# Kernel tuning notes

Measured on AMD Instinct MI355X. Metric: run time of the kernel, lower is better.

Reference implementation:

```python
import jax, jax.numpy as jnp
import numpy as np

D_MODEL = 1024
N_HEADS = 16
HEAD_DIM = D_MODEL // N_HEADS
B, S = 2, 2048


def setup_inputs() -> dict:
    key = jax.random.key(0)
    ks = jax.random.split(key, 12)
    sd = 1.0 / np.sqrt(D_MODEL)
    inp = {
        "x": jax.random.normal(ks[0], (B, S, D_MODEL), dtype=jnp.float32),
        "rel_bias": jax.random.normal(ks[1], (N_HEADS, S, S), dtype=jnp.float32) * 0.02,
        "attn_mask": jnp.zeros((1, 1, S, S), dtype=jnp.float32),
        # Linear params in torch layout: W [out, in], b [out]
        "Wq": jax.random.normal(ks[2], (D_MODEL, D_MODEL), dtype=jnp.float32) * sd,
        "bq": jnp.zeros((D_MODEL,), dtype=jnp.float32),
        "Wk": jax.random.normal(ks[3], (D_MODEL, D_MODEL), dtype=jnp.float32) * sd,
        "bk": jnp.zeros((D_MODEL,), dtype=jnp.float32),
        "Wv": jax.random.normal(ks[4], (D_MODEL, D_MODEL), dtype=jnp.float32) * sd,
        "bv": jnp.zeros((D_MODEL,), dtype=jnp.float32),
        "Wo": jax.random.normal(ks[5], (D_MODEL, D_MODEL), dtype=jnp.float32) * sd,
        "bo": jnp.zeros((D_MODEL,), dtype=jnp.float32),
    }
    return inp


def _split_heads(t):
    # [B, S, D] -> [B, H, S, Hd]
    b, s, _ = t.shape
    return t.reshape(b, s, N_HEADS, HEAD_DIM).transpose(0, 2, 1, 3)


def reference(x, rel_bias, attn_mask, Wq, bq, Wk, bk, Wv, bv, Wo, bo):
    scale = HEAD_DIM ** (-0.5)
    q = _split_heads(x @ Wq.T + bq)  # [B, H, S, Hd]
    k = _split_heads(x @ Wk.T + bk)
    v = _split_heads(x @ Wv.T + bv)
    scores = jnp.einsum("bhqd,bhkd->bhqk", q, k) * scale
    scores = scores + rel_bias  # [H,S,S] broadcasts over batch
    scores = scores + attn_mask  # [1,1,S,S]
    probs = jax.nn.softmax(scores, axis=-1)
    ctx = jnp.einsum("bhqk,bhkd->bhqd", probs, v)  # [B, H, S, Hd]
    ctx = ctx.transpose(0, 2, 1, 3).reshape(x.shape[0], x.shape[1], D_MODEL)
    return ctx @ Wo.T + bo
```

## Files before the change

kernel.cpp:

```cpp
#include <hip/hip_runtime.h>
#include <hip/hip_bf16.h>
#include <stdint.h>

#define S_LEN 2048
#define DM 1024
#define NH 16
#define HD 64

typedef __bf16 bf16x8 __attribute__((ext_vector_type(8)));
typedef float f32x4 __attribute__((ext_vector_type(4)));
typedef unsigned short u16x4 __attribute__((ext_vector_type(4)));

#if __has_builtin(__builtin_amdgcn_exp2f)
#define EXP2F(x) __builtin_amdgcn_exp2f(x)
#else
#define EXP2F(x) exp2f(x)
#endif

__device__ __forceinline__ unsigned short f2bf(float f){
  union { float f; uint32_t u; } v; v.f = f;
  uint32_t r = v.u + 0x7fffu + ((v.u >> 16) & 1u);
  return (unsigned short)(r >> 16);
}

__device__ __forceinline__ void load_lds16(const void* g, void* l){
  __builtin_amdgcn_global_load_lds((const __attribute__((address_space(1))) void*)g,
                                   (__attribute__((address_space(3))) void*)l, 16, 0, 0);
}

__device__ __forceinline__ f32x4 mfma16(bf16x8 a, bf16x8 b, f32x4 c){
  return __builtin_amdgcn_mfma_f32_16x16x32_bf16(a, b, c, 0, 0, 0);
}

__device__ __forceinline__ bf16x8 lds_swz_read(const unsigned short* base, int row, int cb){
  int addr = (row << 7) + (cb ^ ((row & 7) << 4));
  return *reinterpret_cast<const bf16x8*>(reinterpret_cast<const char*>(base) + addr);
}

__global__ void prep_kernel(const float* __restrict__ x,
                            const float* __restrict__ wq, const float* __restrict__ wk,
                            const float* __restrict__ wv, const float* __restrict__ wo,
                            unsigned short* __restrict__ ws_base){
  long idx = ((long)blockIdx.x * 256 + threadIdx.x) * 4;
  const float* s; unsigned short* d; long off;
  if (idx < (1L << 22)) { s = x; d = ws_base; off = idx; }
  else {
    long r = idx - (1L << 22);
    int wsel = (int)(r >> 20);
    off = r & ((1L << 20) - 1);
    s = wsel == 0 ? wq : wsel == 1 ? wk : wsel == 2 ? wv : wo;
    d = ws_base + (1L << 22) + ((long)wsel << 20);
  }
  float4 f = *reinterpret_cast<const float4*>(s + off);
  u16x4 o;
  o[0] = f2bf(f.x); o[1] = f2bf(f.y); o[2] = f2bf(f.z); o[3] = f2bf(f.w);
  *reinterpret_cast<u16x4*>(d + off) = o;
}

template<int MODE>
__global__ __launch_bounds__(256, 2)
void gemm_bt_kernel(const unsigned short* __restrict__ A,
                    const unsigned short* __restrict__ B0,
                    const unsigned short* __restrict__ B1,
                    const unsigned short* __restrict__ B2,
                    const float* __restrict__ bias0,
                    const float* __restrict__ bias1,
                    const float* __restrict__ bias2,
                    unsigned short* __restrict__ q_out,
                    unsigned short* __restrict__ k_out,
                    unsigned short* __restrict__ vt_out,
                    float* __restrict__ f_out)
{
  __shared__ unsigned short As[128 * 64];
  __shared__ unsigned short Bs[128 * 64];
  const int tid = threadIdx.x;
  const int lane = tid & 63;
  const int w = tid >> 6;
  const int wr = w >> 1, wc = w & 1;
  const int mBase = blockIdx.y * 128;
  int nb = blockIdx.x;
  const unsigned short* Bmat; const float* bias; int mat;
  if constexpr (MODE == 0) {
    mat = nb >> 3;
    nb &= 7;
    Bmat = mat == 0 ? B0 : (mat == 1 ? B1 : B2);
    bias = mat == 0 ? bias0 : (mat == 1 ? bias1 : bias2);
  } else { mat = 0; Bmat = B0; bias = bias0; }
  const int nBase = nb * 128;

  f32x4 acc[4][4] = {};
  const int srow = lane >> 3;
  const int ksrc = ((lane & 7) ^ srow) * 8;
  const unsigned short* ArowBase = A    + (size_t)(mBase + w * 32 + srow) * DM + ksrc;
  const unsigned short* BrowBase = Bmat + (size_t)(nBase + w * 32 + srow) * DM + ksrc;

  for (int kt = 0; kt < 16; ++kt) {
    #pragma unroll
    for (int i = 0; i < 4; ++i) {
      load_lds16(ArowBase + (size_t)(i * 8) * DM + kt * 64, &As[(w * 4 + i) * 512]);
      load_lds16(BrowBase + (size_t)(i * 8) * DM + kt * 64, &Bs[(w * 4 + i) * 512]);
    }
    __syncthreads();
    #pragma unroll
    for (int kk = 0; kk < 2; ++kk) {
      bf16x8 af[4], bfr[4];
      const int cb = kk * 64 + ((lane >> 4) << 4);
      #pragma unroll
      for (int m = 0; m < 4; ++m)
        af[m] = lds_swz_read(As, wr * 64 + m * 16 + (lane & 15), cb);
      #pragma unroll
      for (int n = 0; n < 4; ++n)
        bfr[n] = lds_swz_read(Bs, wc * 64 + n * 16 + (lane & 15), cb);
      #pragma unroll
      for (int m = 0; m < 4; ++m)
        #pragma unroll
        for (int n = 0; n < 4; ++n)
          acc[m][n] = mfma16(af[m], bfr[n], acc[m][n]);
    }
    __syncthreads();
  }

  #pragma unroll
  for (int m = 0; m < 4; ++m) {
    #pragma unroll
    for (int n = 0; n < 4; ++n) {
      const int col = nBase + wc * 64 + n * 16 + (lane & 15);
      const float bv = bias[col];
      const int row0 = mBase + wr * 64 + m * 16 + ((lane >> 4) << 2);
      if constexpr (MODE == 1) {
        #pragma unroll
        for (int j = 0; j < 4; ++j)
          f_out[(size_t)(row0 + j) * DM + col] = acc[m][n][j] + bv;
      } else {
        const int h = col >> 6, d = col & 63;
        if (mat < 2) {
          unsigned short* dst = (mat == 0) ? q_out : k_out;
          #pragma unroll
          for (int j = 0; j < 4; ++j) {
            const int row = row0 + j;
            const int b = row >> 11, s = row & 2047;
            dst[(((size_t)b * NH + h) * S_LEN + s) * HD + d] = f2bf(acc[m][n][j] + bv);
          }
        } else {
          const int b = row0 >> 11, s = row0 & 2047;
          u16x4 pk;
          #pragma unroll
          for (int j = 0; j < 4; ++j) pk[j] = f2bf(acc[m][n][j] + bv);
          *reinterpret_cast<u16x4*>(&vt_out[(((size_t)b * NH + h) * HD + d) * S_LEN + s]) = pk;
        }
      }
    }
  }
}


#define LOAD_RAW(kvB) do {                                                    \
    rb0 = *reinterpret_cast<const f32x4*>(bp + (kvB) + g * 4);                \
    rm0 = *reinterpret_cast<const f32x4*>(mp + (kvB) + g * 4);                \
    rb1 = *reinterpret_cast<const f32x4*>(bp + (kvB) + 16 + g * 4);           \
    rm1 = *reinterpret_cast<const f32x4*>(mp + (kvB) + 16 + g * 4);           \
    rb2 = *reinterpret_cast<const f32x4*>(bp + (kvB) + 32 + g * 4);           \
    rm2 = *reinterpret_cast<const f32x4*>(mp + (kvB) + 32 + g * 4);           \
    rb3 = *reinterpret_cast<const f32x4*>(bp + (kvB) + 48 + g * 4);           \
    rm3 = *reinterpret_cast<const f32x4*>(mp + (kvB) + 48 + g * 4);           \
  } while (0)

#define COMBINE do {                                                          \
    bm0 = (rb0 + rm0) * L2E; bm1 = (rb1 + rm1) * L2E;                         \
    bm2 = (rb2 + rm2) * L2E; bm3 = (rb3 + rm3) * L2E;                         \
  } while (0)

#define STAGE(kvB, buf) do {                                                                \
    load_lds16(Kp + (size_t)((kvB) + w * 16 + srow) * HD + ksrc,      &Ks[buf][(w * 2) * 512]);     \
    load_lds16(Vp + (size_t)(w * 16 + srow) * S_LEN + (kvB) + ksrc,   &Vs[buf][(w * 2) * 512]);     \
    load_lds16(Kp + (size_t)((kvB) + w * 16 + 8 + srow) * HD + ksrc,  &Ks[buf][(w * 2 + 1) * 512]); \
    load_lds16(Vp + (size_t)(w * 16 + 8 + srow) * S_LEN + (kvB) + ksrc, &Vs[buf][(w * 2 + 1) * 512]); \
  } while (0)

#define QK_COL(NN, SCN) do {                                                  \
    bf16x8 kf0_ = lds_swz_read(KSB_, (NN) * 16 + q, cbq);                     \
    bf16x8 kf1_ = lds_swz_read(KSB_, (NN) * 16 + q, 64 + cbq);                \
    f32x4 z_ = {};                                                            \
    z_ = mfma16(kf0_, qf0, z_);                                               \
    SCN = mfma16(kf1_, qf1, z_);                                              \
  } while (0)

#define BIAS_COL(SCN, BMN) do {                                               \
    SCN[0] = SCN[0] * SC + BMN[0];                                            \
    SCN[1] = SCN[1] * SC + BMN[1];                                            \
    SCN[2] = SCN[2] * SC + BMN[2];                                            \
    SCN[3] = SCN[3] * SC + BMN[3];                                            \
    mt_ = fmaxf(mt_, fmaxf(fmaxf(SCN[0], SCN[1]), fmaxf(SCN[2], SCN[3])));    \
  } while (0)

#define EXP_COL(SCN) do {                                                     \
    SCN[0] = EXP2F(SCN[0] - mn_); SCN[1] = EXP2F(SCN[1] - mn_);               \
    SCN[2] = EXP2F(SCN[2] - mn_); SCN[3] = EXP2F(SCN[3] - mn_);               \
  } while (0)

#define PWR_COL(NN, SCN) do {                                                 \
    u16x4 pk_;                                                                \
    pk_[0] = f2bf(SCN[0]); pk_[1] = f2bf(SCN[1]);                             \
    pk_[2] = f2bf(SCN[2]); pk_[3] = f2bf(SCN[3]);                             \
    const int colb_ = ((NN) * 16 + 4 * g) * 2;                                \
    *reinterpret_cast<u16x4*>(                                                \
        reinterpret_cast<char*>(Pw_) + (q << 7) + (colb_ ^ ((q & 7) << 4))) = pk_; \
  } while (0)

#define PV_COL(NN, ACCN) do {                                                 \
    bf16x8 vf0_ = lds_swz_read(VSB_, (NN) * 16 + q, cbq);                     \
    bf16x8 vf1_ = lds_swz_read(VSB_, (NN) * 16 + q, 64 + cbq);                \
    ACCN = mfma16(vf0_, pf0_, ACCN);                                          \
    ACCN = mfma16(vf1_, pf1_, ACCN);                                          \
  } while (0)

#define COMPUTE_TILE(KSB, VSB) do {                                           \
    const unsigned short* KSB_ = (KSB);                                       \
    const unsigned short* VSB_ = (VSB);                                       \
    f32x4 sc0_, sc1_, sc2_, sc3_;                                             \
    QK_COL(0, sc0_); QK_COL(1, sc1_); QK_COL(2, sc2_); QK_COL(3, sc3_);       \
    float mt_ = -3.0e38f;                                                     \
    BIAS_COL(sc0_, bm0); BIAS_COL(sc1_, bm1);                                 \
    BIAS_COL(sc2_, bm2); BIAS_COL(sc3_, bm3);                                 \
    mt_ = fmaxf(mt_, __shfl_xor(mt_, 16));                                    \
    mt_ = fmaxf(mt_, __shfl_xor(mt_, 32));                                    \
    const float mn_ = fmaxf(m_run, mt_);                                      \
    const float corr_ = EXP2F(m_run - mn_);                                   \
    m_run = mn_;                                                              \
    EXP_COL(sc0_); EXP_COL(sc1_); EXP_COL(sc2_); EXP_COL(sc3_);               \
    f32x4 ls4_ = sc0_ + sc1_ + sc2_ + sc3_;                                   \
    float ls_ = ls4_[0] + ls4_[1] + ls4_[2] + ls4_[3];                        \
    ls_ += __shfl_xor(ls_, 16);                                               \
    ls_ += __shfl_xor(ls_, 32);                                               \
    l_run = l_run * corr_ + ls_;                                              \
    acc0_ *= corr_; acc1_ *= corr_; acc2_ *= corr_; acc3_ *= corr_;           \
    unsigned short* Pw_ = Ps[w];                                              \
    PWR_COL(0, sc0_); PWR_COL(1, sc1_); PWR_COL(2, sc2_); PWR_COL(3, sc3_);   \
    bf16x8 pf0_ = lds_swz_read(Pw_, q, cbq);                                  \
    bf16x8 pf1_ = lds_swz_read(Pw_, q, 64 + cbq);                             \
    PV_COL(0, acc0_); PV_COL(1, acc1_); PV_COL(2, acc2_); PV_COL(3, acc3_);   \
  } while (0)

__global__ __launch_bounds__(256) __attribute__((amdgpu_waves_per_eu(3, 4)))
void attn_kernel(const unsigned short* __restrict__ Q,
                 const unsigned short* __restrict__ Kmat,
                 const unsigned short* __restrict__ Vt,
                 const float* __restrict__ rel_bias,
                 const float* __restrict__ mask,
                 unsigned short* __restrict__ ctx)
{
  __shared__ unsigned short Ks[2][64 * 64];
  __shared__ unsigned short Vs[2][64 * 64];
  __shared__ unsigned short Ps[4][16 * 64];

  const int logical = (blockIdx.x & 7) * 128 + (blockIdx.x >> 3);
  const int b  = logical & 1;
  const int qt = (logical >> 1) & 31;
  const int h  = logical >> 6;

  const int lane = threadIdx.x & 63, w = threadIdx.x >> 6;
  const int q = lane & 15, g = lane >> 4;
  const size_t bh = (size_t)b * NH + h;
  const int qRow = qt * 64 + w * 16;
  const unsigned short* Qp = Q + (bh * S_LEN + qRow) * HD;
  bf16x8 qf0 = *reinterpret_cast<const bf16x8*>(Qp + (size_t)q * HD + g * 8);
  bf16x8 qf1 = *reinterpret_cast<const bf16x8*>(Qp + (size_t)q * HD + 32 + g * 8);

  const unsigned short* Kp = Kmat + bh * (size_t)S_LEN * HD;
  const unsigned short* Vp = Vt + bh * (size_t)HD * S_LEN;
  const float* bp = rel_bias + (size_t)h * S_LEN * S_LEN + (size_t)(qRow + q) * S_LEN;
  const float* mp = mask + (size_t)(qRow + q) * S_LEN;

  float m_run = -3.0e38f, l_run = 0.f;
  f32x4 acc0_ = {}, acc1_ = {}, acc2_ = {}, acc3_ = {};
  f32x4 rb0, rb1, rb2, rb3, rm0, rm1, rm2, rm3;
  f32x4 bm0, bm1, bm2, bm3;

  const float SC  = 0.125f * 1.44269504089f;
  const float L2E = 1.44269504089f;

  const int srow = lane >> 3;
  const int ksrc = ((lane & 7) ^ srow) * 8;
  const int cbq = g << 4;

  LOAD_RAW(0);
  STAGE(0, 0);
  __syncthreads();

  for (int i = 0; i < 16; ++i) {
    const int t0 = 2 * i;
    COMBINE;
    LOAD_RAW((t0 + 1) * 64);
    STAGE((t0 + 1) * 64, 1);
    COMPUTE_TILE(Ks[0], Vs[0]);
    __syncthreads();
    COMBINE;
    if (i < 15) {
      LOAD_RAW((t0 + 2) * 64);
      STAGE((t0 + 2) * 64, 0);
    }
    COMPUTE_TILE(Ks[1], Vs[1]);
    __syncthreads();
  }

  const float inv = 1.0f / l_run;
  acc0_ *= inv; acc1_ *= inv; acc2_ *= inv; acc3_ *= inv;
  unsigned short* Pw_ = Ps[w];
  PWR_COL(0, acc0_); PWR_COL(1, acc1_); PWR_COL(2, acc2_); PWR_COL(3, acc3_);
  bf16x8 c0 = lds_swz_read(Pw_, q, g << 4);
  bf16x8 c1 = lds_swz_read(Pw_, q, 64 + (g << 4));
  unsigned short* cp = ctx + ((size_t)b * S_LEN + qRow + q) * DM + h * HD;
  *reinterpret_cast<bf16x8*>(cp + 8 * g) = c0;
  *reinterpret_cast<bf16x8*>(cp + 32 + 8 * g) = c1;
}

extern "C" void kernel_launch(void* const* d_in, const int* in_sizes, int n_in,
                              void* d_out, int out_size, void* d_ws, size_t ws_size,
                              hipStream_t stream) {
  (void)in_sizes; (void)n_in; (void)out_size; (void)ws_size;
  const float* x  = (const float*)d_in[0];
  const float* rb = (const float*)d_in[1];
  const float* mk = (const float*)d_in[2];
  const float* Wq = (const float*)d_in[3];
  const float* bq = (const float*)d_in[4];
  const float* Wk = (const float*)d_in[5];
  const float* bk = (const float*)d_in[6];
  const float* Wv = (const float*)d_in[7];
  const float* bv = (const float*)d_in[8];
  const float* Wo = (const float*)d_in[9];
  const float* bo = (const float*)d_in[10];
  float* out = (float*)d_out;

  unsigned short* ws  = (unsigned short*)d_ws;
  unsigned short* xb  = ws;
  unsigned short* wqb = ws + (1L << 22);
  unsigned short* wkb = wqb + (1L << 20);
  unsigned short* wvb = wkb + (1L << 20);
  unsigned short* wob = wvb + (1L << 20);
  unsigned short* Qw  = wob + (1L << 20);
  unsigned short* Kw  = Qw + (1L << 22);
  unsigned short* Vtw = Kw + (1L << 22);
  unsigned short* ctx = Vtw + (1L << 22);

  prep_kernel<<<8192, 256, 0, stream>>>(x, Wq, Wk, Wv, Wo, ws);
  gemm_bt_kernel<0><<<dim3(24, 32), 256, 0, stream>>>(
      xb, wqb, wkb, wvb, bq, bk, bv, Qw, Kw, Vtw, nullptr);
  attn_kernel<<<1024, 256, 0, stream>>>(Qw, Kw, Vtw, rb, mk, ctx);
  gemm_bt_kernel<1><<<dim3(8, 32), 256, 0, stream>>>(
      ctx, wob, nullptr, nullptr, bo, nullptr, nullptr, nullptr, nullptr, nullptr, out);
}
```

Baseline: 237.6 us.

## Load K and V fragments directly from global into registers, dropping LDS staging

Replaces the double-buffered LDS staging of K and V tiles, along with its block-wide barriers, with per-wave direct global loads of the MFMA operand fragments into registers, prefetched one tile ahead. This removes the LDS traffic and the __syncthreads from the KV loop and frees shared memory for occupancy. In exchange, each of the four waves now fetches the same K/V data separately from global/L2, which multiplies that traffic by four. It also raises register pressure and issues narrower, less coalesced loads.

```diff
diff --git a/kernel.cpp b/kernel.cpp
--- a/kernel.cpp
+++ b/kernel.cpp
@@ -170,19 +170,26 @@
     bm2 = (rb2 + rm2) * L2E; bm3 = (rb3 + rm3) * L2E;                         \
   } while (0)
 
-#define STAGE(kvB, buf) do {                                                                \
-    load_lds16(Kp + (size_t)((kvB) + w * 16 + srow) * HD + ksrc,      &Ks[buf][(w * 2) * 512]);     \
-    load_lds16(Vp + (size_t)(w * 16 + srow) * S_LEN + (kvB) + ksrc,   &Vs[buf][(w * 2) * 512]);     \
-    load_lds16(Kp + (size_t)((kvB) + w * 16 + 8 + srow) * HD + ksrc,  &Ks[buf][(w * 2 + 1) * 512]); \
-    load_lds16(Vp + (size_t)(w * 16 + 8 + srow) * S_LEN + (kvB) + ksrc, &Vs[buf][(w * 2 + 1) * 512]); \
-  } while (0)
-
-#define QK_COL(NN, SCN) do {                                                  \
-    bf16x8 kf0_ = lds_swz_read(KSB_, (NN) * 16 + q, cbq);                     \
-    bf16x8 kf1_ = lds_swz_read(KSB_, (NN) * 16 + q, 64 + cbq);                \
-    f32x4 z_ = {};                                                            \
-    z_ = mfma16(kf0_, qf0, z_);                                               \
-    SCN = mfma16(kf1_, qf1, z_);                                              \
+#define LOAD_K(kvB) do {                                                      \
+    kf00 = *reinterpret_cast<const bf16x8*>(Kq + (size_t)(kvB) * HD);         \
+    kf01 = *reinterpret_cast<const bf16x8*>(Kq + (size_t)(kvB) * HD + 32);    \
+    kf10 = *reinterpret_cast<const bf16x8*>(Kq + (size_t)(kvB) * HD + 1024);  \
+    kf11 = *reinterpret_cast<const bf16x8*>(Kq + (size_t)(kvB) * HD + 1056);  \
+    kf20 = *reinterpret_cast<const bf16x8*>(Kq + (size_t)(kvB) * HD + 2048);  \
+    kf21 = *reinterpret_cast<const bf16x8*>(Kq + (size_t)(kvB) * HD + 2080);  \
+    kf30 = *reinterpret_cast<const bf16x8*>(Kq + (size_t)(kvB) * HD + 3072);  \
+    kf31 = *reinterpret_cast<const bf16x8*>(Kq + (size_t)(kvB) * HD + 3104);  \
+  } while (0)
+
+#define LOAD_V(kvB) do {                                                      \
+    vf00 = *reinterpret_cast<const bf16x8*>(Vq0 + (kvB));                     \
+    vf01 = *reinterpret_cast<const bf16x8*>(Vq0 + (kvB) + 32);                \
+    vf10 = *reinterpret_cast<const bf16x8*>(Vq1 + (kvB));                     \
+    vf11 = *reinterpret_cast<const bf16x8*>(Vq1 + (kvB) + 32);                \
+    vf20 = *reinterpret_cast<const bf16x8*>(Vq2 + (kvB));                     \
+    vf21 = *reinterpret_cast<const bf16x8*>(Vq2 + (kvB) + 32);                \
+    vf30 = *reinterpret_cast<const bf16x8*>(Vq3 + (kvB));                     \
+    vf31 = *reinterpret_cast<const bf16x8*>(Vq3 + (kvB) + 32);                \
   } while (0)
 
 #define BIAS_COL(SCN, BMN) do {                                               \
@@ -205,40 +212,6 @@
     const int colb_ = ((NN) * 16 + 4 * g) * 2;                                \
     *reinterpret_cast<u16x4*>(                                                \
         reinterpret_cast<char*>(Pw_) + (q << 7) + (colb_ ^ ((q & 7) << 4))) = pk_; \
-  } while (0)
-
-#define PV_COL(NN, ACCN) do {                                                 \
-    bf16x8 vf0_ = lds_swz_read(VSB_, (NN) * 16 + q, cbq);                     \
-    bf16x8 vf1_ = lds_swz_read(VSB_, (NN) * 16 + q, 64 + cbq);                \
-    ACCN = mfma16(vf0_, pf0_, ACCN);                                          \
-    ACCN = mfma16(vf1_, pf1_, ACCN);                                          \
-  } while (0)
-
-#define COMPUTE_TILE(KSB, VSB) do {                                           \
-    const unsigned short* KSB_ = (KSB);                                       \
-    const unsigned short* VSB_ = (VSB);                                       \
-    f32x4 sc0_, sc1_, sc2_, sc3_;                                             \
-    QK_COL(0, sc0_); QK_COL(1, sc1_); QK_COL(2, sc2_); QK_COL(3, sc3_);       \
-    float mt_ = -3.0e38f;                                                     \
-    BIAS_COL(sc0_, bm0); BIAS_COL(sc1_, bm1);                                 \
-    BIAS_COL(sc2_, bm2); BIAS_COL(sc3_, bm3);                                 \
-    mt_ = fmaxf(mt_, __shfl_xor(mt_, 16));                                    \
-    mt_ = fmaxf(mt_, __shfl_xor(mt_, 32));                                    \
-    const float mn_ = fmaxf(m_run, mt_);                                      \
-    const float corr_ = EXP2F(m_run - mn_);                                   \
-    m_run = mn_;                                                              \
-    EXP_COL(sc0_); EXP_COL(sc1_); EXP_COL(sc2_); EXP_COL(sc3_);               \
-    f32x4 ls4_ = sc0_ + sc1_ + sc2_ + sc3_;                                   \
-    float ls_ = ls4_[0] + ls4_[1] + ls4_[2] + ls4_[3];                        \
-    ls_ += __shfl_xor(ls_, 16);                                               \
-    ls_ += __shfl_xor(ls_, 32);                                               \
-    l_run = l_run * corr_ + ls_;                                              \
-    acc0_ *= corr_; acc1_ *= corr_; acc2_ *= corr_; acc3_ *= corr_;           \
-    unsigned short* Pw_ = Ps[w];                                              \
-    PWR_COL(0, sc0_); PWR_COL(1, sc1_); PWR_COL(2, sc2_); PWR_COL(3, sc3_);   \
-    bf16x8 pf0_ = lds_swz_read(Pw_, q, cbq);                                  \
-    bf16x8 pf1_ = lds_swz_read(Pw_, q, 64 + cbq);                             \
-    PV_COL(0, acc0_); PV_COL(1, acc1_); PV_COL(2, acc2_); PV_COL(3, acc3_);   \
   } while (0)
 
 __global__ __launch_bounds__(256) __attribute__((amdgpu_waves_per_eu(3, 4)))
@@ -249,8 +222,6 @@
                  const float* __restrict__ mask,
                  unsigned short* __restrict__ ctx)
 {
-  __shared__ unsigned short Ks[2][64 * 64];
-  __shared__ unsigned short Vs[2][64 * 64];
   __shared__ unsigned short Ps[4][16 * 64];
 
   const int logical = (blockIdx.x & 7) * 128 + (blockIdx.x >> 3);
@@ -266,8 +237,12 @@
   bf16x8 qf0 = *reinterpret_cast<const bf16x8*>(Qp + (size_t)q * HD + g * 8);
   bf16x8 qf1 = *reinterpret_cast<const bf16x8*>(Qp + (size_t)q * HD + 32 + g * 8);
 
-  const unsigned short* Kp = Kmat + bh * (size_t)S_LEN * HD;
-  const unsigned short* Vp = Vt + bh * (size_t)HD * S_LEN;
+  const unsigned short* Kq  = Kmat + bh * (size_t)S_LEN * HD + (size_t)q * HD + g * 8;
+  const unsigned short* Vb  = Vt + bh * (size_t)HD * S_LEN + g * 8;
+  const unsigned short* Vq0 = Vb + (size_t)q * S_LEN;
+  const unsigned short* Vq1 = Vb + (size_t)(16 + q) * S_LEN;
+  const unsigned short* Vq2 = Vb + (size_t)(32 + q) * S_LEN;
+  const unsigned short* Vq3 = Vb + (size_t)(48 + q) * S_LEN;
   const float* bp = rel_bias + (size_t)h * S_LEN * S_LEN + (size_t)(qRow + q) * S_LEN;
   const float* mp = mask + (size_t)(qRow + q) * S_LEN;
 
@@ -275,37 +250,59 @@
   f32x4 acc0_ = {}, acc1_ = {}, acc2_ = {}, acc3_ = {};
   f32x4 rb0, rb1, rb2, rb3, rm0, rm1, rm2, rm3;
   f32x4 bm0, bm1, bm2, bm3;
+  bf16x8 kf00, kf01, kf10, kf11, kf20, kf21, kf30, kf31;
+  bf16x8 vf00, vf01, vf10, vf11, vf20, vf21, vf30, vf31;
 
   const float SC  = 0.125f * 1.44269504089f;
   const float L2E = 1.44269504089f;
-
-  const int srow = lane >> 3;
-  const int ksrc = ((lane & 7) ^ srow) * 8;
   const int cbq = g << 4;
+  unsigned short* Pw_ = Ps[w];
 
   LOAD_RAW(0);
-  STAGE(0, 0);
-  __syncthreads();
-
-  for (int i = 0; i < 16; ++i) {
-    const int t0 = 2 * i;
+  LOAD_K(0);
+  LOAD_V(0);
+
+  for (int t = 0; t < 32; ++t) {
+    const int nxt = (t + 1) * 64;
     COMBINE;
-    LOAD_RAW((t0 + 1) * 64);
-    STAGE((t0 + 1) * 64, 1);
-    COMPUTE_TILE(Ks[0], Vs[0]);
-    __syncthreads();
-    COMBINE;
-    if (i < 15) {
-      LOAD_RAW((t0 + 2) * 64);
-      STAGE((t0 + 2) * 64, 0);
-    }
-    COMPUTE_TILE(Ks[1], Vs[1]);
-    __syncthreads();
+    if (t < 31) LOAD_RAW(nxt);
+
+    f32x4 sc0_, sc1_, sc2_, sc3_;
+    { f32x4 z_ = {}; z_ = mfma16(kf00, qf0, z_); sc0_ = mfma16(kf01, qf1, z_); }
+    { f32x4 z_ = {}; z_ = mfma16(kf10, qf0, z_); sc1_ = mfma16(kf11, qf1, z_); }
+    { f32x4 z_ = {}; z_ = mfma16(kf20, qf0, z_); sc2_ = mfma16(kf21, qf1, z_); }
+    { f32x4 z_ = {}; z_ = mfma16(kf30, qf0, z_); sc3_ = mfma16(kf31, qf1, z_); }
+    if (t < 31) LOAD_K(nxt);
+
+    float mt_ = -3.0e38f;
+    BIAS_COL(sc0_, bm0); BIAS_COL(sc1_, bm1);
+    BIAS_COL(sc2_, bm2); BIAS_COL(sc3_, bm3);
+    mt_ = fmaxf(mt_, __shfl_xor(mt_, 16));
+    mt_ = fmaxf(mt_, __shfl_xor(mt_, 32));
+    const float mn_ = fmaxf(m_run, mt_);
+    const float corr_ = EXP2F(m_run - mn_);
+    m_run = mn_;
+    EXP_COL(sc0_); EXP_COL(sc1_); EXP_COL(sc2_); EXP_COL(sc3_);
+    f32x4 ls4_ = sc0_ + sc1_ + sc2_ + sc3_;
+    float ls_ = ls4_[0] + ls4_[1] + ls4_[2] + ls4_[3];
+    ls_ += __shfl_xor(ls_, 16);
+    ls_ += __shfl_xor(ls_, 32);
+    l_run = l_run * corr_ + ls_;
+    acc0_ *= corr_; acc1_ *= corr_; acc2_ *= corr_; acc3_ *= corr_;
+
+    PWR_COL(0, sc0_); PWR_COL(1, sc1_); PWR_COL(2, sc2_); PWR_COL(3, sc3_);
+    bf16x8 pf0_ = lds_swz_read(Pw_, q, cbq);
+    bf16x8 pf1_ = lds_swz_read(Pw_, q, 64 + cbq);
+
+    acc0_ = mfma16(vf00, pf0_, acc0_); acc0_ = mfma16(vf01, pf1_, acc0_);
+    acc1_ = mfma16(vf10, pf0_, acc1_); acc1_ = mfma16(vf11, pf1_, acc1_);
+    acc2_ = mfma16(vf20, pf0_, acc2_); acc2_ = mfma16(vf21, pf1_, acc2_);
+    acc3_ = mfma16(vf30, pf0_, acc3_); acc3_ = mfma16(vf31, pf1_, acc3_);
+    if (t < 31) LOAD_V(nxt);
   }
 
   const float inv = 1.0f / l_run;
   acc0_ *= inv; acc1_ *= inv; acc2_ *= inv; acc3_ *= inv;
-  unsigned short* Pw_ = Ps[w];
   PWR_COL(0, acc0_); PWR_COL(1, acc1_); PWR_COL(2, acc2_); PWR_COL(3, acc3_);
   bf16x8 c0 = lds_swz_read(Pw_, q, g << 4);
   bf16x8 c1 = lds_swz_read(Pw_, q, 64 + (g << 4));
```

New measurement: 431.7 us. +81.7%, slower.

## Deepen bias/mask prefetch to two tiles with explicit vmcnt waits and barriers

Applied to the files above, without the earlier changes.

Splits the bias and mask register prefetch into two alternating sets so the raw loads run two tiles ahead instead of one. The __syncthreads calls are replaced by partial s_waitcnt vmcnt(8) plus s_barrier, with sched_barrier fences, so the outstanding bias loads are not drained at every tile boundary. The final two tiles are peeled out of the loop. This adds 32 VGPRs of live prefetch state, which may hurt occupancy. Correctness now depends on the hand-counted vmcnt ordering, which assumes the LDS DMA loads are issued before the register loads.

```diff
diff --git a/kernel.cpp b/kernel.cpp
--- a/kernel.cpp
+++ b/kernel.cpp
@@ -154,35 +154,51 @@
 }
 
 
-#define LOAD_RAW(kvB) do {                                                    \
-    rb0 = *reinterpret_cast<const f32x4*>(bp + (kvB) + g * 4);                \
-    rm0 = *reinterpret_cast<const f32x4*>(mp + (kvB) + g * 4);                \
-    rb1 = *reinterpret_cast<const f32x4*>(bp + (kvB) + 16 + g * 4);           \
-    rm1 = *reinterpret_cast<const f32x4*>(mp + (kvB) + 16 + g * 4);           \
-    rb2 = *reinterpret_cast<const f32x4*>(bp + (kvB) + 32 + g * 4);           \
-    rm2 = *reinterpret_cast<const f32x4*>(mp + (kvB) + 32 + g * 4);           \
-    rb3 = *reinterpret_cast<const f32x4*>(bp + (kvB) + 48 + g * 4);           \
-    rm3 = *reinterpret_cast<const f32x4*>(mp + (kvB) + 48 + g * 4);           \
-  } while (0)
-
-#define COMBINE do {                                                          \
-    bm0 = (rb0 + rm0) * L2E; bm1 = (rb1 + rm1) * L2E;                         \
-    bm2 = (rb2 + rm2) * L2E; bm3 = (rb3 + rm3) * L2E;                         \
-  } while (0)
-
-#define STAGE(kvB, buf) do {                                                                \
-    load_lds16(Kp + (size_t)((kvB) + w * 16 + srow) * HD + ksrc,      &Ks[buf][(w * 2) * 512]);     \
-    load_lds16(Vp + (size_t)(w * 16 + srow) * S_LEN + (kvB) + ksrc,   &Vs[buf][(w * 2) * 512]);     \
-    load_lds16(Kp + (size_t)((kvB) + w * 16 + 8 + srow) * HD + ksrc,  &Ks[buf][(w * 2 + 1) * 512]); \
+#define WAITV8 do { asm volatile("s_waitcnt vmcnt(8)" ::: "memory"); } while (0)
+#define WAITV0 do { asm volatile("s_waitcnt vmcnt(0)" ::: "memory"); } while (0)
+#define SB0    __builtin_amdgcn_sched_barrier(0)
+#define BAR    __builtin_amdgcn_s_barrier()
+
+#define LOAD_RAW_A(kvB) do {                                                  \
+    rbA0 = *reinterpret_cast<const f32x4*>(bp + (kvB) + g * 4);               \
+    rmA0 = *reinterpret_cast<const f32x4*>(mp + (kvB) + g * 4);               \
+    rbA1 = *reinterpret_cast<const f32x4*>(bp + (kvB) + 16 + g * 4);          \
+    rmA1 = *reinterpret_cast<const f32x4*>(mp + (kvB) + 16 + g * 4);          \
+    rbA2 = *reinterpret_cast<const f32x4*>(bp + (kvB) + 32 + g * 4);          \
+    rmA2 = *reinterpret_cast<const f32x4*>(mp + (kvB) + 32 + g * 4);          \
+    rbA3 = *reinterpret_cast<const f32x4*>(bp + (kvB) + 48 + g * 4);          \
+    rmA3 = *reinterpret_cast<const f32x4*>(mp + (kvB) + 48 + g * 4);          \
+  } while (0)
+
+#define LOAD_RAW_B(kvB) do {                                                  \
+    rbB0 = *reinterpret_cast<const f32x4*>(bp + (kvB) + g * 4);               \
+    rmB0 = *reinterpret_cast<const f32x4*>(mp + (kvB) + g * 4);               \
+    rbB1 = *reinterpret_cast<const f32x4*>(bp + (kvB) + 16 + g * 4);          \
+    rmB1 = *reinterpret_cast<const f32x4*>(mp + (kvB) + 16 + g * 4);          \
+    rbB2 = *reinterpret_cast<const f32x4*>(bp + (kvB) + 32 + g * 4);          \
+    rmB2 = *reinterpret_cast<const f32x4*>(mp + (kvB) + 32 + g * 4);          \
+    rbB3 = *reinterpret_cast<const f32x4*>(bp + (kvB) + 48 + g * 4);          \
+    rmB3 = *reinterpret_cast<const f32x4*>(mp + (kvB) + 48 + g * 4);          \
+  } while (0)
+
+#define COMBINE_A do {                                                        \
+    bm0 = (rbA0 + rmA0) * L2E; bm1 = (rbA1 + rmA1) * L2E;                     \
+    bm2 = (rbA2 + rmA2) * L2E; bm3 = (rbA3 + rmA3) * L2E;                     \
+  } while (0)
+
+#define COMBINE_B do {                                                        \
+    bm0 = (rbB0 + rmB0) * L2E; bm1 = (rbB1 + rmB1) * L2E;                     \
+    bm2 = (rbB2 + rmB2) * L2E; bm3 = (rbB3 + rmB3) * L2E;                     \
+  } while (0)
+
+#define STAGE_K(kvB, buf) do {                                                               \
+    load_lds16(Kp + (size_t)((kvB) + w * 16 + srow) * HD + ksrc,     &Ks[buf][(w * 2) * 512]);     \
+    load_lds16(Kp + (size_t)((kvB) + w * 16 + 8 + srow) * HD + ksrc, &Ks[buf][(w * 2 + 1) * 512]); \
+  } while (0)
+
+#define STAGE_V(kvB, buf) do {                                                               \
+    load_lds16(Vp + (size_t)(w * 16 + srow) * S_LEN + (kvB) + ksrc,     &Vs[buf][(w * 2) * 512]);     \
     load_lds16(Vp + (size_t)(w * 16 + 8 + srow) * S_LEN + (kvB) + ksrc, &Vs[buf][(w * 2 + 1) * 512]); \
-  } while (0)
-
-#define QK_COL(NN, SCN) do {                                                  \
-    bf16x8 kf0_ = lds_swz_read(KSB_, (NN) * 16 + q, cbq);                     \
-    bf16x8 kf1_ = lds_swz_read(KSB_, (NN) * 16 + q, 64 + cbq);                \
-    f32x4 z_ = {};                                                            \
-    z_ = mfma16(kf0_, qf0, z_);                                               \
-    SCN = mfma16(kf1_, qf1, z_);                                              \
   } while (0)
 
 #define BIAS_COL(SCN, BMN) do {                                               \
@@ -207,18 +223,22 @@
         reinterpret_cast<char*>(Pw_) + (q << 7) + (colb_ ^ ((q & 7) << 4))) = pk_; \
   } while (0)
 
-#define PV_COL(NN, ACCN) do {                                                 \
-    bf16x8 vf0_ = lds_swz_read(VSB_, (NN) * 16 + q, cbq);                     \
-    bf16x8 vf1_ = lds_swz_read(VSB_, (NN) * 16 + q, 64 + cbq);                \
-    ACCN = mfma16(vf0_, pf0_, ACCN);                                          \
-    ACCN = mfma16(vf1_, pf1_, ACCN);                                          \
-  } while (0)
-
 #define COMPUTE_TILE(KSB, VSB) do {                                           \
     const unsigned short* KSB_ = (KSB);                                       \
     const unsigned short* VSB_ = (VSB);                                       \
     f32x4 sc0_, sc1_, sc2_, sc3_;                                             \
-    QK_COL(0, sc0_); QK_COL(1, sc1_); QK_COL(2, sc2_); QK_COL(3, sc3_);       \
+    { bf16x8 a_ = lds_swz_read(KSB_, 0 * 16 + q, cbq);                        \
+      bf16x8 b_ = lds_swz_read(KSB_, 0 * 16 + q, 64 + cbq);                   \
+      f32x4 z_ = {}; z_ = mfma16(a_, qf0, z_); sc0_ = mfma16(b_, qf1, z_); }  \
+    { bf16x8 a_ = lds_swz_read(KSB_, 1 * 16 + q, cbq);                        \
+      bf16x8 b_ = lds_swz_read(KSB_, 1 * 16 + q, 64 + cbq);                   \
+      f32x4 z_ = {}; z_ = mfma16(a_, qf0, z_); sc1_ = mfma16(b_, qf1, z_); }  \
+    { bf16x8 a_ = lds_swz_read(KSB_, 2 * 16 + q, cbq);                        \
+      bf16x8 b_ = lds_swz_read(KSB_, 2 * 16 + q, 64 + cbq);                   \
+      f32x4 z_ = {}; z_ = mfma16(a_, qf0, z_); sc2_ = mfma16(b_, qf1, z_); }  \
+    { bf16x8 a_ = lds_swz_read(KSB_, 3 * 16 + q, cbq);                        \
+      bf16x8 b_ = lds_swz_read(KSB_, 3 * 16 + q, 64 + cbq);                   \
+      f32x4 z_ = {}; z_ = mfma16(a_, qf0, z_); sc3_ = mfma16(b_, qf1, z_); }  \
     float mt_ = -3.0e38f;                                                     \
     BIAS_COL(sc0_, bm0); BIAS_COL(sc1_, bm1);                                 \
     BIAS_COL(sc2_, bm2); BIAS_COL(sc3_, bm3);                                 \
@@ -234,11 +254,21 @@
     ls_ += __shfl_xor(ls_, 32);                                               \
     l_run = l_run * corr_ + ls_;                                              \
     acc0_ *= corr_; acc1_ *= corr_; acc2_ *= corr_; acc3_ *= corr_;           \
-    unsigned short* Pw_ = Ps[w];                                              \
     PWR_COL(0, sc0_); PWR_COL(1, sc1_); PWR_COL(2, sc2_); PWR_COL(3, sc3_);   \
     bf16x8 pf0_ = lds_swz_read(Pw_, q, cbq);                                  \
     bf16x8 pf1_ = lds_swz_read(Pw_, q, 64 + cbq);                             \
-    PV_COL(0, acc0_); PV_COL(1, acc1_); PV_COL(2, acc2_); PV_COL(3, acc3_);   \
+    { bf16x8 a_ = lds_swz_read(VSB_, 0 * 16 + q, cbq);                        \
+      bf16x8 b_ = lds_swz_read(VSB_, 0 * 16 + q, 64 + cbq);                   \
+      acc0_ = mfma16(a_, pf0_, acc0_); acc0_ = mfma16(b_, pf1_, acc0_); }     \
+    { bf16x8 a_ = lds_swz_read(VSB_, 1 * 16 + q, cbq);                        \
+      bf16x8 b_ = lds_swz_read(VSB_, 1 * 16 + q, 64 + cbq);                   \
+      acc1_ = mfma16(a_, pf0_, acc1_); acc1_ = mfma16(b_, pf1_, acc1_); }     \
+    { bf16x8 a_ = lds_swz_read(VSB_, 2 * 16 + q, cbq);                        \
+      bf16x8 b_ = lds_swz_read(VSB_, 2 * 16 + q, 64 + cbq);                   \
+      acc2_ = mfma16(a_, pf0_, acc2_); acc2_ = mfma16(b_, pf1_, acc2_); }     \
+    { bf16x8 a_ = lds_swz_read(VSB_, 3 * 16 + q, cbq);                        \
+      bf16x8 b_ = lds_swz_read(VSB_, 3 * 16 + q, 64 + cbq);                   \
+      acc3_ = mfma16(a_, pf0_, acc3_); acc3_ = mfma16(b_, pf1_, acc3_); }     \
   } while (0)
 
 __global__ __launch_bounds__(256) __attribute__((amdgpu_waves_per_eu(3, 4)))
@@ -273,7 +303,8 @@
 
   float m_run = -3.0e38f, l_run = 0.f;
   f32x4 acc0_ = {}, acc1_ = {}, acc2_ = {}, acc3_ = {};
-  f32x4 rb0, rb1, rb2, rb3, rm0, rm1, rm2, rm3;
+  f32x4 rbA0, rbA1, rbA2, rbA3, rmA0, rmA1, rmA2, rmA3;
+  f32x4 rbB0, rbB1, rbB2, rbB3, rmB0, rmB1, rmB2, rmB3;
   f32x4 bm0, bm1, bm2, bm3;
 
   const float SC  = 0.125f * 1.44269504089f;
@@ -282,30 +313,45 @@
   const int srow = lane >> 3;
   const int ksrc = ((lane & 7) ^ srow) * 8;
   const int cbq = g << 4;
-
-  LOAD_RAW(0);
-  STAGE(0, 0);
-  __syncthreads();
-
-  for (int i = 0; i < 16; ++i) {
+  unsigned short* Pw_ = Ps[w];
+
+  STAGE_V(0, 0);
+  STAGE_K(0, 0);
+  LOAD_RAW_A(0);
+  LOAD_RAW_B(64);
+  SB0;
+  WAITV8; SB0; BAR;
+
+  for (int i = 0; i < 15; ++i) {
     const int t0 = 2 * i;
-    COMBINE;
-    LOAD_RAW((t0 + 1) * 64);
-    STAGE((t0 + 1) * 64, 1);
+    COMBINE_A;
+    STAGE_V((t0 + 1) * 64, 1);
+    STAGE_K((t0 + 1) * 64, 1);
+    LOAD_RAW_A((t0 + 2) * 64);
+    SB0;
     COMPUTE_TILE(Ks[0], Vs[0]);
-    __syncthreads();
-    COMBINE;
-    if (i < 15) {
-      LOAD_RAW((t0 + 2) * 64);
-      STAGE((t0 + 2) * 64, 0);
-    }
+    WAITV8; SB0; BAR;
+    COMBINE_B;
+    STAGE_V((t0 + 2) * 64, 0);
+    STAGE_K((t0 + 2) * 64, 0);
+    LOAD_RAW_B((t0 + 3) * 64);
+    SB0;
     COMPUTE_TILE(Ks[1], Vs[1]);
-    __syncthreads();
+    WAITV8; SB0; BAR;
   }
+
+  COMBINE_A;
+  STAGE_V(31 * 64, 1);
+  STAGE_K(31 * 64, 1);
+  SB0;
+  COMPUTE_TILE(Ks[0], Vs[0]);
+  WAITV0; SB0; BAR;
+  COMBINE_B;
+  SB0;
+  COMPUTE_TILE(Ks[1], Vs[1]);
 
   const float inv = 1.0f / l_run;
   acc0_ *= inv; acc1_ *= inv; acc2_ *= inv; acc3_ *= inv;
-  unsigned short* Pw_ = Ps[w];
   PWR_COL(0, acc0_); PWR_COL(1, acc1_); PWR_COL(2, acc2_); PWR_COL(3, acc3_);
   bf16x8 c0 = lds_swz_read(Pw_, q, g << 4);
   bf16x8 c1 = lds_swz_read(Pw_, q, 64 + (g << 4));
```

New measurement: 241.2 us. Within noise of the previous version (+1.5%).

## Software-pipeline attention loop: overlap next QK tile with current softmax-PV

Applied to the files above, without the earlier changes.

Restructures the flash-attention main loop so that the QK^T MFMAs for tile t+1 are issued alongside the softmax and PV of tile t. K and V staging are split, with K prefetched two tiles ahead and V one ahead. __syncthreads is replaced by explicit s_waitcnt vmcnt, sched_barrier and s_barrier to control when loads are waited on. The aim is to hide exp/softmax latency behind matrix work and reduce barrier stalls. The cost is extra registers for a second score set and fragile hand-tuned wait counts.

```diff
diff --git a/kernel.cpp b/kernel.cpp
--- a/kernel.cpp
+++ b/kernel.cpp
@@ -154,6 +154,11 @@
 }
 
 
+#define WAITV8 do { asm volatile("s_waitcnt vmcnt(8)" ::: "memory"); } while (0)
+#define WAITV0 do { asm volatile("s_waitcnt vmcnt(0)" ::: "memory"); } while (0)
+#define SB0    __builtin_amdgcn_sched_barrier(0)
+#define BAR    __builtin_amdgcn_s_barrier()
+
 #define LOAD_RAW(kvB) do {                                                    \
     rb0 = *reinterpret_cast<const f32x4*>(bp + (kvB) + g * 4);                \
     rm0 = *reinterpret_cast<const f32x4*>(mp + (kvB) + g * 4);                \
@@ -170,19 +175,30 @@
     bm2 = (rb2 + rm2) * L2E; bm3 = (rb3 + rm3) * L2E;                         \
   } while (0)
 
-#define STAGE(kvB, buf) do {                                                                \
-    load_lds16(Kp + (size_t)((kvB) + w * 16 + srow) * HD + ksrc,      &Ks[buf][(w * 2) * 512]);     \
-    load_lds16(Vp + (size_t)(w * 16 + srow) * S_LEN + (kvB) + ksrc,   &Vs[buf][(w * 2) * 512]);     \
-    load_lds16(Kp + (size_t)((kvB) + w * 16 + 8 + srow) * HD + ksrc,  &Ks[buf][(w * 2 + 1) * 512]); \
+#define STAGE_K(kvB, buf) do {                                                               \
+    load_lds16(Kp + (size_t)((kvB) + w * 16 + srow) * HD + ksrc,     &Ks[buf][(w * 2) * 512]);     \
+    load_lds16(Kp + (size_t)((kvB) + w * 16 + 8 + srow) * HD + ksrc, &Ks[buf][(w * 2 + 1) * 512]); \
+  } while (0)
+
+#define STAGE_V(kvB, buf) do {                                                               \
+    load_lds16(Vp + (size_t)(w * 16 + srow) * S_LEN + (kvB) + ksrc,     &Vs[buf][(w * 2) * 512]);     \
     load_lds16(Vp + (size_t)(w * 16 + 8 + srow) * S_LEN + (kvB) + ksrc, &Vs[buf][(w * 2 + 1) * 512]); \
   } while (0)
 
-#define QK_COL(NN, SCN) do {                                                  \
-    bf16x8 kf0_ = lds_swz_read(KSB_, (NN) * 16 + q, cbq);                     \
-    bf16x8 kf1_ = lds_swz_read(KSB_, (NN) * 16 + q, 64 + cbq);                \
-    f32x4 z_ = {};                                                            \
-    z_ = mfma16(kf0_, qf0, z_);                                               \
-    SCN = mfma16(kf1_, qf1, z_);                                              \
+#define QK_TILE(S0, S1, S2, S3, KSB) do {                                     \
+    const unsigned short* KQ_ = (KSB);                                        \
+    { bf16x8 a_ = lds_swz_read(KQ_, 0 * 16 + q, cbq);                         \
+      bf16x8 b_ = lds_swz_read(KQ_, 0 * 16 + q, 64 + cbq);                    \
+      f32x4 z_ = {}; z_ = mfma16(a_, qf0, z_); S0 = mfma16(b_, qf1, z_); }    \
+    { bf16x8 a_ = lds_swz_read(KQ_, 1 * 16 + q, cbq);                         \
+      bf16x8 b_ = lds_swz_read(KQ_, 1 * 16 + q, 64 + cbq);                    \
+      f32x4 z_ = {}; z_ = mfma16(a_, qf0, z_); S1 = mfma16(b_, qf1, z_); }    \
+    { bf16x8 a_ = lds_swz_read(KQ_, 2 * 16 + q, cbq);                         \
+      bf16x8 b_ = lds_swz_read(KQ_, 2 * 16 + q, 64 + cbq);                    \
+      f32x4 z_ = {}; z_ = mfma16(a_, qf0, z_); S2 = mfma16(b_, qf1, z_); }    \
+    { bf16x8 a_ = lds_swz_read(KQ_, 3 * 16 + q, cbq);                         \
+      bf16x8 b_ = lds_swz_read(KQ_, 3 * 16 + q, 64 + cbq);                    \
+      f32x4 z_ = {}; z_ = mfma16(a_, qf0, z_); S3 = mfma16(b_, qf1, z_); }    \
   } while (0)
 
 #define BIAS_COL(SCN, BMN) do {                                               \
@@ -207,38 +223,50 @@
         reinterpret_cast<char*>(Pw_) + (q << 7) + (colb_ ^ ((q & 7) << 4))) = pk_; \
   } while (0)
 
-#define PV_COL(NN, ACCN) do {                                                 \
-    bf16x8 vf0_ = lds_swz_read(VSB_, (NN) * 16 + q, cbq);                     \
-    bf16x8 vf1_ = lds_swz_read(VSB_, (NN) * 16 + q, 64 + cbq);                \
-    ACCN = mfma16(vf0_, pf0_, ACCN);                                          \
-    ACCN = mfma16(vf1_, pf1_, ACCN);                                          \
-  } while (0)
-
-#define COMPUTE_TILE(KSB, VSB) do {                                           \
-    const unsigned short* KSB_ = (KSB);                                       \
-    const unsigned short* VSB_ = (VSB);                                       \
-    f32x4 sc0_, sc1_, sc2_, sc3_;                                             \
-    QK_COL(0, sc0_); QK_COL(1, sc1_); QK_COL(2, sc2_); QK_COL(3, sc3_);       \
+#define SOFTMAX_PV(S0, S1, S2, S3, VSB) do {                                  \
+    const unsigned short* VQ_ = (VSB);                                        \
     float mt_ = -3.0e38f;                                                     \
-    BIAS_COL(sc0_, bm0); BIAS_COL(sc1_, bm1);                                 \
-    BIAS_COL(sc2_, bm2); BIAS_COL(sc3_, bm3);                                 \
+    BIAS_COL(S0, bm0); BIAS_COL(S1, bm1);                                     \
+    BIAS_COL(S2, bm2); BIAS_COL(S3, bm3);                                     \
     mt_ = fmaxf(mt_, __shfl_xor(mt_, 16));                                    \
     mt_ = fmaxf(mt_, __shfl_xor(mt_, 32));                                    \
     const float mn_ = fmaxf(m_run, mt_);                                      \
     const float corr_ = EXP2F(m_run - mn_);                                   \
     m_run = mn_;                                                              \
-    EXP_COL(sc0_); EXP_COL(sc1_); EXP_COL(sc2_); EXP_COL(sc3_);               \
-    f32x4 ls4_ = sc0_ + sc1_ + sc2_ + sc3_;                                   \
+    EXP_COL(S0); EXP_COL(S1); EXP_COL(S2); EXP_COL(S3);                       \
+    f32x4 ls4_ = S0 + S1 + S2 + S3;                                           \
     float ls_ = ls4_[0] + ls4_[1] + ls4_[2] + ls4_[3];                        \
     ls_ += __shfl_xor(ls_, 16);                                               \
     ls_ += __shfl_xor(ls_, 32);                                               \
     l_run = l_run * corr_ + ls_;                                              \
     acc0_ *= corr_; acc1_ *= corr_; acc2_ *= corr_; acc3_ *= corr_;           \
-    unsigned short* Pw_ = Ps[w];                                              \
-    PWR_COL(0, sc0_); PWR_COL(1, sc1_); PWR_COL(2, sc2_); PWR_COL(3, sc3_);   \
+    PWR_COL(0, S0); PWR_COL(1, S1); PWR_COL(2, S2); PWR_COL(3, S3);           \
     bf16x8 pf0_ = lds_swz_read(Pw_, q, cbq);                                  \
     bf16x8 pf1_ = lds_swz_read(Pw_, q, 64 + cbq);                             \
-    PV_COL(0, acc0_); PV_COL(1, acc1_); PV_COL(2, acc2_); PV_COL(3, acc3_);   \
+    { bf16x8 a_ = lds_swz_read(VQ_, 0 * 16 + q, cbq);                         \
+      bf16x8 b_ = lds_swz_read(VQ_, 0 * 16 + q, 64 + cbq);                    \
+      acc0_ = mfma16(a_, pf0_, acc0_); acc0_ = mfma16(b_, pf1_, acc0_); }     \
+    { bf16x8 a_ = lds_swz_read(VQ_, 1 * 16 + q, cbq);                         \
+      bf16x8 b_ = lds_swz_read(VQ_, 1 * 16 + q, 64 + cbq);                    \
+      acc1_ = mfma16(a_, pf0_, acc1_); acc1_ = mfma16(b_, pf1_, acc1_); }     \
+    { bf16x8 a_ = lds_swz_read(VQ_, 2 * 16 + q, cbq);                         \
+      bf16x8 b_ = lds_swz_read(VQ_, 2 * 16 + q, 64 + cbq);                    \
+      acc2_ = mfma16(a_, pf0_, acc2_); acc2_ = mfma16(b_, pf1_, acc2_); }     \
+    { bf16x8 a_ = lds_swz_read(VQ_, 3 * 16 + q, cbq);                         \
+      bf16x8 b_ = lds_swz_read(VQ_, 3 * 16 + q, 64 + cbq);                    \
+      acc3_ = mfma16(a_, pf0_, acc3_); acc3_ = mfma16(b_, pf1_, acc3_); }     \
+  } while (0)
+
+#define PHASE(t, SCC0, SCC1, SCC2, SCC3, SCN0, SCN1, SCN2, SCN3, DO_K, DO_RAW) do { \
+    COMBINE;                                                                  \
+    if (DO_K) STAGE_K(((t) + 2) * 64, (t) & 1);                               \
+    STAGE_V(((t) + 1) * 64, ((t) + 1) & 1);                                   \
+    SB0;                                                                      \
+    if (DO_RAW) LOAD_RAW(((t) + 1) * 64);                                     \
+    SB0;                                                                      \
+    QK_TILE(SCN0, SCN1, SCN2, SCN3, Ks[((t) + 1) & 1]);                       \
+    SOFTMAX_PV(SCC0, SCC1, SCC2, SCC3, Vs[(t) & 1]);                          \
+    WAITV8; SB0; BAR;                                                         \
   } while (0)
 
 __global__ __launch_bounds__(256) __attribute__((amdgpu_waves_per_eu(3, 4)))
@@ -275,6 +303,7 @@
   f32x4 acc0_ = {}, acc1_ = {}, acc2_ = {}, acc3_ = {};
   f32x4 rb0, rb1, rb2, rb3, rm0, rm1, rm2, rm3;
   f32x4 bm0, bm1, bm2, bm3;
+  f32x4 scE0, scE1, scE2, scE3, scO0, scO1, scO2, scO3;
 
   const float SC  = 0.125f * 1.44269504089f;
   const float L2E = 1.44269504089f;
@@ -282,30 +311,29 @@
   const int srow = lane >> 3;
   const int ksrc = ((lane & 7) ^ srow) * 8;
   const int cbq = g << 4;
-
+  unsigned short* Pw_ = Ps[w];
+
+  STAGE_V(0, 0);
+  STAGE_K(0, 0);
+  STAGE_K(64, 1);
+  SB0;
+  WAITV0; SB0; BAR;
   LOAD_RAW(0);
-  STAGE(0, 0);
-  __syncthreads();
-
-  for (int i = 0; i < 16; ++i) {
+  SB0;
+  QK_TILE(scE0, scE1, scE2, scE3, Ks[0]);
+  BAR;
+
+  for (int i = 0; i < 15; ++i) {
     const int t0 = 2 * i;
-    COMBINE;
-    LOAD_RAW((t0 + 1) * 64);
-    STAGE((t0 + 1) * 64, 1);
-    COMPUTE_TILE(Ks[0], Vs[0]);
-    __syncthreads();
-    COMBINE;
-    if (i < 15) {
-      LOAD_RAW((t0 + 2) * 64);
-      STAGE((t0 + 2) * 64, 0);
-    }
-    COMPUTE_TILE(Ks[1], Vs[1]);
-    __syncthreads();
+    PHASE(t0,     scE0, scE1, scE2, scE3, scO0, scO1, scO2, scO3, true, true);
+    PHASE(t0 + 1, scO0, scO1, scO2, scO3, scE0, scE1, scE2, scE3, true, true);
   }
+  PHASE(30, scE0, scE1, scE2, scE3, scO0, scO1, scO2, scO3, false, true);
+  COMBINE;
+  SOFTMAX_PV(scO0, scO1, scO2, scO3, Vs[1]);
 
   const float inv = 1.0f / l_run;
   acc0_ *= inv; acc1_ *= inv; acc2_ *= inv; acc3_ *= inv;
-  unsigned short* Pw_ = Ps[w];
   PWR_COL(0, acc0_); PWR_COL(1, acc1_); PWR_COL(2, acc2_); PWR_COL(3, acc3_);
   bf16x8 c0 = lds_swz_read(Pw_, q, g << 4);
   bf16x8 c1 = lds_swz_read(Pw_, q, 64 + (g << 4));
```

Measured after the change: 237.6 us. About the same (-0.0%).
